# Optimization experiments

Measured on AMD Instinct MI355X. Metric: run time of the kernel, lower is better.

The kernel has to match this reference:

```python
import jax, jax.numpy as jnp
import numpy as np

GRID = (32, 32, 32)
LOWER = jnp.array([0.0, 0.0, 0.0], jnp.float32)
UPPER = jnp.array([1.0, 1.0, 1.0], jnp.float32)
B = 16
N = 131072
C_IN = 1018          # per-point feature channels; +3 offset +3 xyz = 1024 = nn_channels[0]
D_IN = 1024
C_OUT = 128          # nn_channels[-1]
BN_EPS = 1e-5


def setup_inputs() -> dict:
    key = jax.random.key(0)
    ks = jax.random.split(key, 8)
    W1 = jax.random.normal(ks[5], (D_IN, C_OUT), jnp.float32) / np.sqrt(D_IN).astype(np.float32)
    return {
        "xyz": jax.random.uniform(ks[0], (N, 3), jnp.float32),
        "pred_nocs": jax.random.uniform(ks[1], (N, 3), jnp.float32),
        "per_point_features": jax.random.normal(ks[2], (N, C_IN), jnp.float32),
        "pred_confidence": jax.random.uniform(ks[3], (N, 1), jnp.float32),
        "batch_idx": jnp.sort(jax.random.randint(ks[4], (N,), 0, B, dtype=jnp.int32)),
        "batch_size": B,
        "W1": W1,
        "b1": jnp.zeros((C_OUT,), jnp.float32),
        "g1": jnp.ones((C_OUT,), jnp.float32),
        "be1": jnp.zeros((C_OUT,), jnp.float32),
    }


def _batchnorm_train(x, gamma, beta):
    # torch BatchNorm1d in training mode: biased variance over the batch dim
    m = jnp.mean(x, axis=0)
    v = jnp.mean(jnp.square(x - m), axis=0)
    return (x - m) * jax.lax.rsqrt(v + BN_EPS) * gamma + beta


def reference(xyz, pred_nocs, per_point_features, pred_confidence, batch_idx,
              batch_size, W1, b1, g1, be1):
    gs_f = jnp.array(GRID, jnp.float32)
    gs_i = jnp.array(GRID, jnp.int32)
    # VirtualGrid.get_points_grid_idxs: round to nearest cell, clip into grid
    idx_f = jnp.round((pred_nocs - LOWER) / (UPPER - LOWER) * (gs_f - 1.0))
    idx = jnp.clip(idx_f.astype(jnp.int32), 0, gs_i - 1)  # [N,3]
    # VirtualGrid.idxs_to_points
    grid_pts = idx.astype(jnp.float32) / (gs_f - 1.0) * (UPPER - LOWER) + LOWER
    local_offset = pred_nocs - grid_pts
    feats = jnp.concatenate([per_point_features, local_offset, xyz], axis=-1)  # [N,1024]
    # local_nn: Linear -> ReLU -> PointBatchNorm1D
    h = _batchnorm_train(jax.nn.relu(feats @ W1 + b1), g1, be1)  # [N,128]
    # flatten (b,i,j,k) -> flat grid index
    gx, gy, gz = GRID
    flat = ((batch_idx.astype(jnp.int32) * gx + idx[:, 0]) * gy + idx[:, 1]) * gz + idx[:, 2]
    num_grids = batch_size * gx * gy * gz
    ssum = jax.ops.segment_sum(h, flat, num_segments=num_grids)          # [num_grids,128]
    cnt = jax.ops.segment_sum(jnp.ones((h.shape[0], 1), h.dtype), flat, num_segments=num_grids)
    mean = ssum / jnp.maximum(cnt, 1.0)  # empty cells stay 0 (torch_scatter mean)
    # [num_grids, C] -> [B, gx, gy, gz, C] -> [B, C, gx, gy, gz]
    vol = mean.reshape(batch_size, gx, gy, gz, C_OUT).transpose(0, 4, 1, 2, 3)
    return vol
```

## Files before the change

kernel.cpp:

```cpp
#include <hip/hip_runtime.h>

#define NPTS   131072
#define CIN    1018
#define DIN    1024
#define COUT   128
#define BB     16
#define GDIM   32
#define NCELLS (BB*GDIM*GDIM*GDIM)
#define NREP   8

typedef float          f32x4  __attribute__((ext_vector_type(4)));
typedef __bf16         bf16x8 __attribute__((ext_vector_type(8)));
typedef unsigned short us8    __attribute__((ext_vector_type(8)));

__device__ __forceinline__ unsigned short f2bf(float f) {
    union { float f; unsigned u; } v; v.f = f;
    unsigned r = v.u + 0x7FFFu + ((v.u >> 16) & 1u);
    return (unsigned short)(r >> 16);
}

__device__ __forceinline__ us8 cvt8f(f32x4 lo, f32x4 hi) {
    bf16x8 r;
    r[0] = (__bf16)lo[0]; r[1] = (__bf16)lo[1]; r[2] = (__bf16)lo[2]; r[3] = (__bf16)lo[3];
    r[4] = (__bf16)hi[0]; r[5] = (__bf16)hi[1]; r[6] = (__bf16)hi[2]; r[7] = (__bf16)hi[3];
    return __builtin_bit_cast(us8, r);
}

__device__ __forceinline__ f32x4 MF(us8 a, us8 b, f32x4 c) {
    return __builtin_amdgcn_mfma_f32_16x16x32_bf16(
        __builtin_bit_cast(bf16x8, a), __builtin_bit_cast(bf16x8, b), c, 0, 0, 0);
}

__global__ __launch_bounds__(256) void k_zero(int4* __restrict__ p, int n4) {
    const int idx = blockIdx.x * 256 + threadIdx.x;
    const int4 z = {0, 0, 0, 0};
    for (int i = idx; i < n4; i += 131072) p[i] = z;
}

__global__ __launch_bounds__(256) void k_packW(const float* __restrict__ W1,
                                               unsigned short* __restrict__ pw) {
    const int t  = blockIdx.x * 256 + threadIdx.x;
    const int l  = t & 63;
    const int cb = (t >> 6) & 7;
    const int ks = t >> 9;
    const int col  = cb * 16 + (l & 15);
    const int krow = ks * 32 + ((l >> 4) * 8);
    unsigned short* dst = pw + (size_t)t * 8;
#pragma unroll
    for (int i = 0; i < 8; ++i) dst[i] = f2bf(W1[(size_t)(krow + i) * COUT + col]);
}

__global__ __launch_bounds__(256) void k_prep(const float* __restrict__ xyz,
                                              const float* __restrict__ nocs,
                                              const float* __restrict__ feats,
                                              const int*   __restrict__ bidx,
                                              float* __restrict__ tail,
                                              int*   __restrict__ cellid,
                                              int*   __restrict__ cnt) {
    const int i = blockIdx.x * 256 + threadIdx.x;
    if (i >= NPTS) return;
    int id[3]; float off[3];
#pragma unroll
    for (int d = 0; d < 3; ++d) {
        const float nv = nocs[i * 3 + d];
        int ii = (int)rintf(nv * 31.0f);
        ii = ii < 0 ? 0 : (ii > 31 ? 31 : ii);
        id[d]  = ii;
        off[d] = nv - (float)ii / 31.0f;
    }
    float* tl = tail + (size_t)i * 8;
    tl[0] = feats[(size_t)i * CIN + 1016];
    tl[1] = feats[(size_t)i * CIN + 1017];
    tl[2] = off[0]; tl[3] = off[1]; tl[4] = off[2];
    tl[5] = xyz[i*3+0]; tl[6] = xyz[i*3+1]; tl[7] = xyz[i*3+2];
    const int cell = ((bidx[i] * GDIM + id[0]) * GDIM + id[1]) * GDIM + id[2];
    cellid[i] = cell;
    atomicAdd(&cnt[cell], 1);
}

__global__ __launch_bounds__(256) void k_scanA(const int* __restrict__ cnt,
                                               int* __restrict__ rel,
                                               int* __restrict__ bsum) {
    __shared__ int wtot[4], woff[4];
    const int t = threadIdx.x, blk = blockIdx.x;
    const int4 c4 = *(const int4*)&cnt[blk * 1024 + t * 4];
    const int s = c4.x + c4.y + c4.z + c4.w;
    int v = s;
    const int lane = t & 63, w = t >> 6;
#pragma unroll
    for (int d = 1; d < 64; d <<= 1) {
        const int u = __shfl_up(v, d);
        if (lane >= d) v += u;
    }
    if (lane == 63) wtot[w] = v;
    __syncthreads();
    if (t == 0) {
        int a = 0;
#pragma unroll
        for (int i = 0; i < 4; ++i) { woff[i] = a; a += wtot[i]; }
        bsum[blk] = a;
    }
    __syncthreads();
    const int excl = woff[w] + v - s;
    int* r = rel + blk * 1024 + t * 4;
    r[0] = excl; r[1] = excl + c4.x;
    r[2] = excl + c4.x + c4.y; r[3] = excl + c4.x + c4.y + c4.z;
}

__global__ __launch_bounds__(256) void k_scanB(const int* __restrict__ bsum,
                                               int* __restrict__ boff) {
    __shared__ int wtot[4], woff[4];
    const int t = threadIdx.x;
    const int2 c2 = *(const int2*)&bsum[t * 2];
    const int s = c2.x + c2.y;
    int v = s;
    const int lane = t & 63, w = t >> 6;
#pragma unroll
    for (int d = 1; d < 64; d <<= 1) {
        const int u = __shfl_up(v, d);
        if (lane >= d) v += u;
    }
    if (lane == 63) wtot[w] = v;
    __syncthreads();
    if (t == 0) {
        int a = 0;
#pragma unroll
        for (int i = 0; i < 4; ++i) { woff[i] = a; a += wtot[i]; }
    }
    __syncthreads();
    const int excl = woff[w] + v - s;
    boff[t * 2] = excl; boff[t * 2 + 1] = excl + c2.x;
}

__global__ __launch_bounds__(256) void k_fill(const int* __restrict__ cellid,
                                              const int* __restrict__ rel,
                                              const int* __restrict__ boff,
                                              int* __restrict__ cursor,
                                              int* __restrict__ dstrow) {
    const int i = blockIdx.x * 256 + threadIdx.x;
    if (i >= NPTS) return;
    const int cell = cellid[i];
    const int slot = atomicAdd(&cursor[cell], 1);
    dstrow[i] = rel[cell] + boff[cell >> 10] + slot;
}


template<int DIRECT>
__global__ void k_gemm(const float* __restrict__ feats,
                       const float* __restrict__ tail,
                       const int*   __restrict__ dstrow,
                       const float* __restrict__ b1,
                       const unsigned short* __restrict__ pw,
                       float* __restrict__ dst,
                       float* __restrict__ gstats) {
    __shared__ float S[3 * 12288];
    const int t = threadIdx.x;
    const int w = t >> 6, l = t & 63;
    const int kgrp = l >> 4, l15 = l & 15;
    const int row0b = blockIdx.x * 128;
    const int swz = l15 & 7;
    const int lr = w * 16 + l15;

    f32x4 acc[8];
#pragma unroll
    for (int cb = 0; cb < 8; ++cb) {
#pragma unroll
        for (int d = 0; d < 4; ++d) acc[cb][d] = 0.f;
    }

#define STAGE6(stg, ch) do{                                               \
    float* _base = S + (stg) * 12288;                                     \
    _Pragma("unroll")                                                     \
    for (int _i = 0; _i < 4; ++_i) {            \
        const int _s   = t + _i * 512;                                    \
        const int _row = _s >> 4;                                         \
        const int _c4  = (_s & 15) ^ (_row & 7);                          \
        const int _k   = (ch) * 64 + _c4 * 4;                             \
        const float* _src = (_k < 1016)                                   \
            ? feats + (size_t)(row0b + _row) * CIN + _k                   \
            : tail  + (size_t)(row0b + _row) * 8 + (_k - 1016);           \
        __builtin_amdgcn_global_load_lds(                                 \
            (const __attribute__((address_space(1))) void*)_src,          \
            (__attribute__((address_space(3))) void*)&_base[_s * 4],      \
            16, 0, 0);                                                    \
    }                                                                     \
    _Pragma("unroll")                                                     \
    for (int _i = 0; _i < 2; ++_i) {            \
        const int _s = t + _i * 512;                                      \
        __builtin_amdgcn_global_load_lds(                                 \
            (const __attribute__((address_space(1))) void*)                \
                (pw + (size_t)(ch) * 8192 + (size_t)_s * 8),              \
            (__attribute__((address_space(3))) void*)&_base[8192 + _s*4], \
            16, 0, 0);                                                    \
    }                                                                     \
}while(0)

    STAGE6(0, 0);
    STAGE6(1, 1);
    int cur = 0, nxt2 = 2;
    for (int ch = 0; ch < 16; ++ch) {
        __builtin_amdgcn_sched_barrier(0);
        if (ch == 15) asm volatile("s_waitcnt vmcnt(0)" ::: "memory");
        else          asm volatile("s_waitcnt vmcnt(6)" ::: "memory");
        __builtin_amdgcn_sched_barrier(0);
        __builtin_amdgcn_s_barrier();
        __builtin_amdgcn_sched_barrier(0);
        if (ch + 2 < 16) STAGE6(nxt2, ch + 2);
        const float* bufA = S + cur * 12288;
        const unsigned short* bufB = (const unsigned short*)(bufA + 8192);
#pragma unroll
        for (int ks = 0; ks < 2; ++ks) {
            const int c4a = ks * 8 + kgrp * 2;
            const f32x4 lo = *(const f32x4*)&bufA[lr * 64 + (( c4a      ^ swz) << 2)];
            const f32x4 hi = *(const f32x4*)&bufA[lr * 64 + (((c4a + 1) ^ swz) << 2)];
            const us8 a = cvt8f(lo, hi);
#pragma unroll
            for (int cb = 0; cb < 8; ++cb) {
                const us8 b = *(const us8*)(bufB + (((ks * 8 + cb) * 64) + l) * 8);
                acc[cb] = MF(a, b, acc[cb]);
            }
        }
        __builtin_amdgcn_sched_barrier(0);
        cur  = cur  == 2 ? 0 : cur + 1;
        nxt2 = nxt2 == 2 ? 0 : nxt2 + 1;
    }
#undef STAGE6

    int r0[4];
#pragma unroll
    for (int j = 0; j < 4; ++j)
        r0[j] = dstrow[row0b + w * 16 + kgrp * 4 + j];
    float* grep = gstats + (size_t)((blockIdx.x * 8 + w) & (NREP - 1)) * 256;
#pragma unroll
    for (int cb = 0; cb < 8; ++cb) {
        const int c = cb * 16 + l15;
        const float bias = b1[c];
        float s = 0.f, q = 0.f;
#pragma unroll
        for (int j = 0; j < 4; ++j) {
            float v0 = acc[cb][j] + bias; v0 = v0 > 0.f ? v0 : 0.f;
            if (DIRECT) {
                const int a = r0[j];
                unsafeAtomicAdd(dst + (((size_t)((a >> 15) * COUT + c)) << 15) + (a & 32767), v0);
            } else {
                dst[(size_t)r0[j] * COUT + c] = v0;
            }
            s += v0; q += v0 * v0;
        }
        s += __shfl_xor(s, 16); s += __shfl_xor(s, 32);
        q += __shfl_xor(q, 16); q += __shfl_xor(q, 32);
        if (l < 16) {
            unsafeAtomicAdd(grep + c, s);
            unsafeAtomicAdd(grep + COUT + c, q);
        }
    }
}

__global__ void k_stats(const float* __restrict__ gstats, const float* __restrict__ g1,
                        const float* __restrict__ be1, float* __restrict__ ss) {
    const int c = threadIdx.x;
    float sm = 0.f, sq = 0.f;
#pragma unroll
    for (int r = 0; r < NREP; ++r) {
        sm += gstats[r * 256 + c];
        sq += gstats[r * 256 + COUT + c];
    }
    const float invn = 1.0f / (float)NPTS;
    const float mean = sm * invn;
    float var = sq * invn - mean * mean;
    var = var < 0.f ? 0.f : var;
    const float sc = g1[c] * rsqrtf(var + 1e-5f);
    ss[c] = sc;
    ss[COUT + c] = be1[c] - mean * sc;
}

__global__ __launch_bounds__(256) void k_out(const float* __restrict__ h,
                                             const int* __restrict__ cnt,
                                             const int* __restrict__ rel,
                                             const int* __restrict__ boff,
                                             const float* __restrict__ ss,
                                             float* __restrict__ out) {
    __shared__ float tile[128 * 128];
    __shared__ float linv[128];
    __shared__ float lss[256];
    const int t  = threadIdx.x;
    const int s0 = blockIdx.x * 128;
    const int b = s0 >> 15, sp0 = s0 & 32767;
    const int boff0 = boff[s0 >> 10];
    if (t < 128) {
        const int cn = cnt[s0 + t];
        linv[t] = cn > 0 ? 1.0f / (float)cn : 0.f;
    } else {
        const int c = t - 128;
        lss[c] = ss[c]; lss[128 + c] = ss[COUT + c];
    }
    const int q = t & 31, r8 = t >> 5;
#pragma unroll
    for (int rep = 0; rep < 16; ++rep) {
        const int j = r8 + rep * 8;
        const int cj = cnt[s0 + j];
        if (cj > 0) {
            const int st = rel[s0 + j] + boff0;
            f32x4 v; v[0] = v[1] = v[2] = v[3] = 0.f;
            for (int k = 0; k < cj; ++k) {
                const f32x4 hv = *(const f32x4*)&h[(size_t)(st + k) * COUT + q * 4];
                v[0] += hv[0]; v[1] += hv[1]; v[2] += hv[2]; v[3] += hv[3];
            }
#pragma unroll
            for (int d = 0; d < 4; ++d) {
                const int c = q * 4 + d;
                tile[c * 128 + (j ^ (c & 28))] = v[d];
            }
        }
    }
    __syncthreads();
#pragma unroll
    for (int p = 0; p < 16; ++p) {
        const int c = p * 8 + r8;
        const float sc = lss[c], sh = lss[128 + c];
        const int u = c & 28;
        const f32x4 vv = *(const f32x4*)&tile[c * 128 + ((q * 4) ^ u)];
        f32x4 o;
#pragma unroll
        for (int d = 0; d < 4; ++d) {
            const float inv = linv[q * 4 + d];
            o[d] = inv > 0.f ? vv[d] * inv * sc + sh : 0.f;
        }
        *(f32x4*)&out[(((size_t)(b * COUT + c)) << 15) + sp0 + q * 4] = o;
    }
}

__global__ __launch_bounds__(256) void k_norm_inplace(float* __restrict__ out,
                                                      const int* __restrict__ cnt,
                                                      const float* __restrict__ ss,
                                                      size_t total) {
    const size_t i = ((size_t)blockIdx.x * 256 + threadIdx.x) * 4;
    if (i >= total) return;
    const int c = (int)((i >> 15) & 127);
    const size_t cellb = ((i >> 22) << 15) | (i & 32767);
    f32x4 v = *(f32x4*)&out[i];
    const int4 cn = *(const int4*)&cnt[cellb];
    const float sc = ss[c], sh = ss[COUT + c];
    const int cna[4] = {cn.x, cn.y, cn.z, cn.w};
#pragma unroll
    for (int d = 0; d < 4; ++d)
        v[d] = cna[d] > 0 ? v[d] / (float)cna[d] * sc + sh : 0.f;
    *(f32x4*)&out[i] = v;
}

extern "C" void kernel_launch(void* const* d_in, const int* in_sizes, int n_in,
                              void* d_out, int out_size, void* d_ws, size_t ws_size,
                              hipStream_t stream) {
    const float* xyz   = (const float*)d_in[0];
    const float* nocs  = (const float*)d_in[1];
    const float* feats = (const float*)d_in[2];
    const int*   bidx  = (const int*)d_in[4];
    const float* W1    = (const float*)d_in[6];
    const float* b1    = (const float*)d_in[7];
    const float* g1    = (const float*)d_in[8];
    const float* be1   = (const float*)d_in[9];
    float* out = (float*)d_out;
    float* ws  = (float*)d_ws;

    const size_t HF  = (size_t)NPTS * COUT;
    const size_t STF = NREP * 256;
    const size_t oA_h    = 0;
    const size_t oA_cnt  = HF;
    const size_t oA_cur  = oA_cnt + NCELLS;
    const size_t oA_st   = oA_cur + NCELLS;
    const size_t oA_rel  = oA_st + STF;
    const size_t oA_bof  = oA_rel + NCELLS;
    const size_t oA_dr   = oA_bof + 512;
    const size_t oA_ss   = oA_dr + NPTS;
    const size_t oA_tail = oA_ss + 256;
    const size_t oA_cid  = oA_tail + (size_t)NPTS * 8;
    const size_t oA_pw   = oA_cid + NPTS;
    const size_t needA   = (oA_pw + 65536) * sizeof(float);
    const bool planA = ws_size >= needA;

    const size_t oB_cnt = 0, oB_st = NCELLS, oB_ss = oB_st + STF,
                 oB_tail = oB_ss + 256, oB_cid = oB_tail + (size_t)NPTS * 8,
                 oB_pw = oB_cid + NPTS;

    float* h   = planA ? ws + oA_h : nullptr;
    int*   cnt = (int*)(ws + (planA ? oA_cnt : oB_cnt));
    int*   cur = planA ? (int*)(ws + oA_cur) : nullptr;
    float* st  = ws + (planA ? oA_st : oB_st);
    int*   rel = planA ? (int*)(ws + oA_rel) : nullptr;
    int*   bof = planA ? (int*)(ws + oA_bof) : nullptr;
    int*   dr  = planA ? (int*)(ws + oA_dr) : nullptr;
    float* ssb = ws + (planA ? oA_ss : oB_ss);
    float* tl  = ws + (planA ? oA_tail : oB_tail);
    int*   cid = (int*)(ws + (planA ? oA_cid : oB_cid));
    unsigned short* pw = (unsigned short*)(ws + (planA ? oA_pw : oB_pw));

    if (planA) {
        k_zero<<<512, 256, 0, stream>>>((int4*)cnt, (int)((2 * NCELLS + STF) / 4));
    } else {
        k_zero<<<512, 256, 0, stream>>>((int4*)cnt, (int)((NCELLS + STF) / 4));
        hipMemsetAsync(out, 0, (size_t)out_size * sizeof(float), stream);
    }

    k_packW<<<64, 256, 0, stream>>>(W1, pw);
    k_prep<<<NPTS / 256, 256, 0, stream>>>(xyz, nocs, feats, bidx, tl, cid, cnt);
    if (planA) {
        k_scanA<<<512, 256, 0, stream>>>(cnt, rel, bof);
        k_scanB<<<1, 256, 0, stream>>>(bof, bof);
        k_fill<<<NPTS / 256, 256, 0, stream>>>(cid, rel, bof, cur, dr);
        k_gemm<0><<<NPTS / 128, 512, 0, stream>>>(feats, tl, dr, b1, pw, h, st);
        k_stats<<<1, 128, 0, stream>>>(st, g1, be1, ssb);
        k_out<<<NCELLS / 128, 256, 0, stream>>>(h, cnt, rel, bof, ssb, out);
    } else {
        k_gemm<1><<<NPTS / 128, 512, 0, stream>>>(feats, tl, cid, b1, pw, out, st);
        k_stats<<<1, 128, 0, stream>>>(st, g1, be1, ssb);
        const size_t total = (size_t)out_size;
        k_norm_inplace<<<(unsigned)((total + 1023) / 1024), 256, 0, stream>>>(out, cnt, ssb, total);
    }
    (void)in_sizes; (void)n_in; (void)d_in;
}
```

Before: 346.6 us.

## Stage GEMM tiles through registers instead of direct global-to-LDS loads

Replaces the global_load_lds async copies with plain global loads into a two-deep register ring, then explicit LDS stores, and fully unrolls the 16-chunk loop with a 3-slot LDS buffer. The goal is to avoid the constraints and latency of the direct-to-LDS path and let the compiler overlap register loads with the MFMA work. In exchange it costs extra VGPRs for the staged data, which can lower occupancy, and adds LDS store instructions. It also replaces the vmcnt waits with waits on the LDS writes.

```diff
diff --git a/kernel.cpp b/kernel.cpp
--- a/kernel.cpp
+++ b/kernel.cpp
@@ -161,6 +161,14 @@
     const int swz = l15 & 7;
     const int lr = w * 16 + l15;
 
+    int arow[4], ac4[4];
+#pragma unroll
+    for (int i = 0; i < 4; ++i) {
+        const int s = t + i * 512;
+        arow[i] = s >> 4;
+        ac4[i]  = ((s & 15) ^ ((s >> 4) & 7)) * 4;
+    }
+
     f32x4 acc[8];
 #pragma unroll
     for (int cb = 0; cb < 8; ++cb) {
@@ -168,45 +176,52 @@
         for (int d = 0; d < 4; ++d) acc[cb][d] = 0.f;
     }
 
-#define STAGE6(stg, ch) do{                                               \
-    float* _base = S + (stg) * 12288;                                     \
+    f32x4 Ra[2][4];
+    us8   Rb[2][2];
+
+#define LOADR(p, ch) do{                                                  \
     _Pragma("unroll")                                                     \
-    for (int _i = 0; _i < 4; ++_i) {            \
-        const int _s   = t + _i * 512;                                    \
-        const int _row = _s >> 4;                                         \
-        const int _c4  = (_s & 15) ^ (_row & 7);                          \
-        const int _k   = (ch) * 64 + _c4 * 4;                             \
+    for (int _i = 0; _i < 4; ++_i) {                                      \
+        const int _k = (ch) * 64 + ac4[_i];                               \
         const float* _src = (_k < 1016)                                   \
-            ? feats + (size_t)(row0b + _row) * CIN + _k                   \
-            : tail  + (size_t)(row0b + _row) * 8 + (_k - 1016);           \
-        __builtin_amdgcn_global_load_lds(                                 \
-            (const __attribute__((address_space(1))) void*)_src,          \
-            (__attribute__((address_space(3))) void*)&_base[_s * 4],      \
-            16, 0, 0);                                                    \
+            ? feats + (size_t)(row0b + arow[_i]) * CIN + _k               \
+            : tail  + (size_t)(row0b + arow[_i]) * 8 + (_k - 1016);       \
+        Ra[p][_i] = *(const f32x4*)_src;                                  \
     }                                                                     \
     _Pragma("unroll")                                                     \
-    for (int _i = 0; _i < 2; ++_i) {            \
-        const int _s = t + _i * 512;                                      \
-        __builtin_amdgcn_global_load_lds(                                 \
-            (const __attribute__((address_space(1))) void*)                \
-                (pw + (size_t)(ch) * 8192 + (size_t)_s * 8),              \
-            (__attribute__((address_space(3))) void*)&_base[8192 + _s*4], \
-            16, 0, 0);                                                    \
-    }                                                                     \
+    for (int _i = 0; _i < 2; ++_i)                                        \
+        Rb[p][_i] = *(const us8*)(pw + (size_t)(ch) * 8192 +              \
+                                  ((size_t)(t + _i * 512)) * 8);          \
 }while(0)
 
-    STAGE6(0, 0);
-    STAGE6(1, 1);
-    int cur = 0, nxt2 = 2;
+#define WRITES(p, stg) do{                                                \
+    float* _b = S + (stg) * 12288;                                        \
+    _Pragma("unroll")                                                     \
+    for (int _i = 0; _i < 4; ++_i)                                        \
+        *(f32x4*)&_b[(t + _i * 512) * 4] = Ra[p][_i];                     \
+    _Pragma("unroll")                                                     \
+    for (int _i = 0; _i < 2; ++_i)                                        \
+        *(us8*)&_b[8192 + (t + _i * 512) * 4] = Rb[p][_i];                \
+}while(0)
+
+    LOADR(0, 0);
+    __builtin_amdgcn_sched_barrier(0);
+    LOADR(1, 1);
+    __builtin_amdgcn_sched_barrier(0);
+    WRITES(0, 0);
+    asm volatile("s_waitcnt lgkmcnt(0)" ::: "memory");
+    __builtin_amdgcn_s_barrier();
+    __builtin_amdgcn_sched_barrier(0);
+
+#pragma unroll
     for (int ch = 0; ch < 16; ++ch) {
+        if (ch + 2 < 16) LOADR(ch & 1, ch + 2);
         __builtin_amdgcn_sched_barrier(0);
-        if (ch == 15) asm volatile("s_waitcnt vmcnt(0)" ::: "memory");
-        else          asm volatile("s_waitcnt vmcnt(6)" ::: "memory");
-        __builtin_amdgcn_sched_barrier(0);
+        if (ch + 1 < 16) WRITES((ch + 1) & 1, (ch + 1) % 3);
+        asm volatile("s_waitcnt lgkmcnt(0)" ::: "memory");
         __builtin_amdgcn_s_barrier();
         __builtin_amdgcn_sched_barrier(0);
-        if (ch + 2 < 16) STAGE6(nxt2, ch + 2);
-        const float* bufA = S + cur * 12288;
+        const float* bufA = S + (ch % 3) * 12288;
         const unsigned short* bufB = (const unsigned short*)(bufA + 8192);
 #pragma unroll
         for (int ks = 0; ks < 2; ++ks) {
@@ -221,10 +236,9 @@
             }
         }
         __builtin_amdgcn_sched_barrier(0);
-        cur  = cur  == 2 ? 0 : cur + 1;
-        nxt2 = nxt2 == 2 ? 0 : nxt2 + 1;
-    }
-#undef STAGE6
+    }
+#undef LOADR
+#undef WRITES
 
     int r0[4];
 #pragma unroll
```

Result: slower. 368.3 us (+6.3%).

## Restructure GEMM to 16-row tiles with bf16 A in LDS and register-held W

Applied to the files above, without the earlier changes.

Replaces the 128-row, 512-thread pipelined GEMM with a 16-row-per-block kernel. Each block reads its contiguous feature span once, converts it to bf16 and stores it swizzled in LDS. Each wave then computes 32 output channels, streaming W fragments from global memory into registers with double buffering. The tail buffer now holds only the offset and xyz values, since the last two feature columns come from the contiguous span. This removes the multistage LDS pipeline and the per-iteration conversions, but W is re-read by many more blocks (8192 instead of 1024) and global loads are no longer overlapped through LDS.

```diff
diff --git a/kernel.cpp b/kernel.cpp
--- a/kernel.cpp
+++ b/kernel.cpp
@@ -17,13 +17,6 @@
     union { float f; unsigned u; } v; v.f = f;
     unsigned r = v.u + 0x7FFFu + ((v.u >> 16) & 1u);
     return (unsigned short)(r >> 16);
-}
-
-__device__ __forceinline__ us8 cvt8f(f32x4 lo, f32x4 hi) {
-    bf16x8 r;
-    r[0] = (__bf16)lo[0]; r[1] = (__bf16)lo[1]; r[2] = (__bf16)lo[2]; r[3] = (__bf16)lo[3];
-    r[4] = (__bf16)hi[0]; r[5] = (__bf16)hi[1]; r[6] = (__bf16)hi[2]; r[7] = (__bf16)hi[3];
-    return __builtin_bit_cast(us8, r);
 }
 
 __device__ __forceinline__ f32x4 MF(us8 a, us8 b, f32x4 c) {
@@ -52,7 +45,6 @@
 
 __global__ __launch_bounds__(256) void k_prep(const float* __restrict__ xyz,
                                               const float* __restrict__ nocs,
-                                              const float* __restrict__ feats,
                                               const int*   __restrict__ bidx,
                                               float* __restrict__ tail,
                                               int*   __restrict__ cellid,
@@ -69,10 +61,9 @@
         off[d] = nv - (float)ii / 31.0f;
     }
     float* tl = tail + (size_t)i * 8;
-    tl[0] = feats[(size_t)i * CIN + 1016];
-    tl[1] = feats[(size_t)i * CIN + 1017];
-    tl[2] = off[0]; tl[3] = off[1]; tl[4] = off[2];
-    tl[5] = xyz[i*3+0]; tl[6] = xyz[i*3+1]; tl[7] = xyz[i*3+2];
+    tl[0] = off[0]; tl[1] = off[1]; tl[2] = off[2];
+    tl[3] = xyz[i*3+0]; tl[4] = xyz[i*3+1]; tl[5] = xyz[i*3+2];
+    tl[6] = 0.f; tl[7] = 0.f;
     const int cell = ((bidx[i] * GDIM + id[0]) * GDIM + id[1]) * GDIM + id[2];
     cellid[i] = cell;
     atomicAdd(&cnt[cell], 1);
@@ -146,104 +137,84 @@
 
 
 template<int DIRECT>
-__global__ void k_gemm(const float* __restrict__ feats,
-                       const float* __restrict__ tail,
-                       const int*   __restrict__ dstrow,
-                       const float* __restrict__ b1,
-                       const unsigned short* __restrict__ pw,
-                       float* __restrict__ dst,
-                       float* __restrict__ gstats) {
-    __shared__ float S[3 * 12288];
+__global__ __launch_bounds__(256) void k_gemm2(const float* __restrict__ feats,
+                                               const float* __restrict__ tail,
+                                               const int*   __restrict__ dstrow,
+                                               const float* __restrict__ b1,
+                                               const unsigned short* __restrict__ pw,
+                                               float* __restrict__ dst,
+                                               float* __restrict__ gstats) {
+    __shared__ unsigned As[16 * 512];
     const int t = threadIdx.x;
     const int w = t >> 6, l = t & 63;
     const int kgrp = l >> 4, l15 = l & 15;
-    const int row0b = blockIdx.x * 128;
-    const int swz = l15 & 7;
-    const int lr = w * 16 + l15;
-
-    f32x4 acc[8];
-#pragma unroll
-    for (int cb = 0; cb < 8; ++cb) {
-#pragma unroll
-        for (int d = 0; d < 4; ++d) acc[cb][d] = 0.f;
-    }
-
-#define STAGE6(stg, ch) do{                                               \
-    float* _base = S + (stg) * 12288;                                     \
+    const int row0 = blockIdx.x * 16;
+
+    const float2* span = (const float2*)(feats + (size_t)row0 * CIN);
+    for (int f = t; f < 8144; f += 256) {
+        const float2 v = span[f];
+        const unsigned r16 = (unsigned)f / 509u;
+        const int k2 = f - (int)r16 * 509;
+        const unsigned pk = (unsigned)f2bf(v.x) | ((unsigned)f2bf(v.y) << 16);
+        const int slot = (k2 >> 2) ^ (int)(r16 & 7u);
+        As[(int)r16 * 512 + slot * 4 + (k2 & 3)] = pk;
+    }
+    if (t < 96) {
+        const int r = t / 6, d = t - r * 6;
+        const int k = 1018 + d;
+        const int slot = 127 ^ (r & 7);
+        ((unsigned short*)As)[r * 1024 + slot * 8 + (k & 7)] = f2bf(tail[(size_t)(row0 + r) * 8 + d]);
+    }
+    __syncthreads();
+
+    f32x4 acc[2];
+#pragma unroll
+    for (int cbb = 0; cbb < 2; ++cbb) { acc[cbb][0]=0.f; acc[cbb][1]=0.f; acc[cbb][2]=0.f; acc[cbb][3]=0.f; }
+    us8 BX[2][2], BY[2][2];
+
+#define LOADB2(B, ch) do{                                                 \
     _Pragma("unroll")                                                     \
-    for (int _i = 0; _i < 4; ++_i) {            \
-        const int _s   = t + _i * 512;                                    \
-        const int _row = _s >> 4;                                         \
-        const int _c4  = (_s & 15) ^ (_row & 7);                          \
-        const int _k   = (ch) * 64 + _c4 * 4;                             \
-        const float* _src = (_k < 1016)                                   \
-            ? feats + (size_t)(row0b + _row) * CIN + _k                   \
-            : tail  + (size_t)(row0b + _row) * 8 + (_k - 1016);           \
-        __builtin_amdgcn_global_load_lds(                                 \
-            (const __attribute__((address_space(1))) void*)_src,          \
-            (__attribute__((address_space(3))) void*)&_base[_s * 4],      \
-            16, 0, 0);                                                    \
-    }                                                                     \
-    _Pragma("unroll")                                                     \
-    for (int _i = 0; _i < 2; ++_i) {            \
-        const int _s = t + _i * 512;                                      \
-        __builtin_amdgcn_global_load_lds(                                 \
-            (const __attribute__((address_space(1))) void*)                \
-                (pw + (size_t)(ch) * 8192 + (size_t)_s * 8),              \
-            (__attribute__((address_space(3))) void*)&_base[8192 + _s*4], \
-            16, 0, 0);                                                    \
-    }                                                                     \
+    for (int _ks = 0; _ks < 2; ++_ks)                                     \
+        _Pragma("unroll")                                                 \
+        for (int _cbb = 0; _cbb < 2; ++_cbb)                              \
+            B[_ks][_cbb] = *(const us8*)(pw +                             \
+                ((((ch)*2 + _ks)*8 + (w*2 + _cbb))*64 + l)*8);            \
 }while(0)
 
-    STAGE6(0, 0);
-    STAGE6(1, 1);
-    int cur = 0, nxt2 = 2;
+    LOADB2(BX, 0);
+#pragma unroll
     for (int ch = 0; ch < 16; ++ch) {
-        __builtin_amdgcn_sched_barrier(0);
-        if (ch == 15) asm volatile("s_waitcnt vmcnt(0)" ::: "memory");
-        else          asm volatile("s_waitcnt vmcnt(6)" ::: "memory");
-        __builtin_amdgcn_sched_barrier(0);
-        __builtin_amdgcn_s_barrier();
-        __builtin_amdgcn_sched_barrier(0);
-        if (ch + 2 < 16) STAGE6(nxt2, ch + 2);
-        const float* bufA = S + cur * 12288;
-        const unsigned short* bufB = (const unsigned short*)(bufA + 8192);
+        if (ch + 1 < 16) { if (ch & 1) LOADB2(BX, ch + 1); else LOADB2(BY, ch + 1); }
+        const us8 (*cur)[2] = (ch & 1) ? BY : BX;
 #pragma unroll
         for (int ks = 0; ks < 2; ++ks) {
-            const int c4a = ks * 8 + kgrp * 2;
-            const f32x4 lo = *(const f32x4*)&bufA[lr * 64 + (( c4a      ^ swz) << 2)];
-            const f32x4 hi = *(const f32x4*)&bufA[lr * 64 + (((c4a + 1) ^ swz) << 2)];
-            const us8 a = cvt8f(lo, hi);
-#pragma unroll
-            for (int cb = 0; cb < 8; ++cb) {
-                const us8 b = *(const us8*)(bufB + (((ks * 8 + cb) * 64) + l) * 8);
-                acc[cb] = MF(a, b, acc[cb]);
-            }
-        }
-        __builtin_amdgcn_sched_barrier(0);
-        cur  = cur  == 2 ? 0 : cur + 1;
-        nxt2 = nxt2 == 2 ? 0 : nxt2 + 1;
-    }
-#undef STAGE6
-
-    int r0[4];
+            const int g = ch * 8 + ks * 4 + kgrp;
+            const int slot = g ^ (l15 & 7);
+            const us8 a = *(const us8*)&As[l15 * 512 + slot * 4];
+            acc[0] = MF(a, cur[ks][0], acc[0]);
+            acc[1] = MF(a, cur[ks][1], acc[1]);
+        }
+    }
+#undef LOADB2
+
+    int rr[4];
 #pragma unroll
     for (int j = 0; j < 4; ++j)
-        r0[j] = dstrow[row0b + w * 16 + kgrp * 4 + j];
-    float* grep = gstats + (size_t)((blockIdx.x * 8 + w) & (NREP - 1)) * 256;
-#pragma unroll
-    for (int cb = 0; cb < 8; ++cb) {
-        const int c = cb * 16 + l15;
+        rr[j] = dstrow[row0 + kgrp * 4 + j];
+    float* grep = gstats + (size_t)((blockIdx.x * 4 + w) & (NREP - 1)) * 256;
+#pragma unroll
+    for (int cbb = 0; cbb < 2; ++cbb) {
+        const int c = w * 32 + cbb * 16 + l15;
         const float bias = b1[c];
         float s = 0.f, q = 0.f;
 #pragma unroll
         for (int j = 0; j < 4; ++j) {
-            float v0 = acc[cb][j] + bias; v0 = v0 > 0.f ? v0 : 0.f;
+            float v0 = acc[cbb][j] + bias; v0 = v0 > 0.f ? v0 : 0.f;
             if (DIRECT) {
-                const int a = r0[j];
+                const int a = rr[j];
                 unsafeAtomicAdd(dst + (((size_t)((a >> 15) * COUT + c)) << 15) + (a & 32767), v0);
             } else {
-                dst[(size_t)r0[j] * COUT + c] = v0;
+                dst[(size_t)rr[j] * COUT + c] = v0;
             }
             s += v0; q += v0 * v0;
         }
@@ -402,16 +373,16 @@
     }
 
     k_packW<<<64, 256, 0, stream>>>(W1, pw);
-    k_prep<<<NPTS / 256, 256, 0, stream>>>(xyz, nocs, feats, bidx, tl, cid, cnt);
+    k_prep<<<NPTS / 256, 256, 0, stream>>>(xyz, nocs, bidx, tl, cid, cnt);
     if (planA) {
         k_scanA<<<512, 256, 0, stream>>>(cnt, rel, bof);
         k_scanB<<<1, 256, 0, stream>>>(bof, bof);
         k_fill<<<NPTS / 256, 256, 0, stream>>>(cid, rel, bof, cur, dr);
-        k_gemm<0><<<NPTS / 128, 512, 0, stream>>>(feats, tl, dr, b1, pw, h, st);
+        k_gemm2<0><<<NPTS / 16, 256, 0, stream>>>(feats, tl, dr, b1, pw, h, st);
         k_stats<<<1, 128, 0, stream>>>(st, g1, be1, ssb);
         k_out<<<NCELLS / 128, 256, 0, stream>>>(h, cnt, rel, bof, ssb, out);
     } else {
-        k_gemm<1><<<NPTS / 128, 512, 0, stream>>>(feats, tl, cid, b1, pw, out, st);
+        k_gemm2<1><<<NPTS / 16, 256, 0, stream>>>(feats, tl, cid, b1, pw, out, st);
         k_stats<<<1, 128, 0, stream>>>(st, g1, be1, ssb);
         const size_t total = (size_t)out_size;
         k_norm_inplace<<<(unsigned)((total + 1023) / 1024), 256, 0, stream>>>(out, cnt, ssb, total);
```

Result: slower. 389.7 us (+12.4%).
